# Kernel optimization log

Measured on AMD Instinct MI355X. Metric: run time of the kernel, lower is better.

Reference implementation:

```python
import jax, jax.numpy as jnp
import numpy as np

ALPHAS = [0.1, 0.3, 0.5]
WEIGHTS = [0.5, 0.3, 0.2]


def setup_inputs() -> dict:
    key = jax.random.key(0)
    k1, k2 = jax.random.split(key)
    pred = jax.random.normal(k1, (64, 4096, 64), dtype=jnp.float32)
    target = jax.random.normal(k2, (64, 4096, 64), dtype=jnp.float32)
    return {"pred": pred, "target": target}


def _ema(x, alpha):
    # x: [B, T, D]; EMA along axis 1: y0 = x0, y_t = alpha*x_t + (1-alpha)*y_{t-1}
    x0 = x[:, 0]                      # [B, D]
    xs = jnp.moveaxis(x[:, 1:], 1, 0)  # [T-1, B, D] for scan over time

    def step(carry, xt):
        y = alpha * xt + (1.0 - alpha) * carry
        return y, y

    _, ys = jax.lax.scan(step, x0, xs)  # [T-1, B, D]
    return jnp.concatenate([x0[:, None], jnp.moveaxis(ys, 0, 1)], axis=1)


def reference(pred, target):
    loss = None
    for alpha, weight in zip(ALPHAS, WEIGHTS):
        pe = _ema(pred, alpha)
        te = _ema(target, alpha)
        mse = jnp.mean((pe - te) ** 2, axis=1)  # [B, D]
        term = weight * mse
        loss = term if loss is None else loss + term
    return jnp.mean(loss)  # reduction='mean'
```

## Files before the change

kernel.cpp:

```cpp
#include <hip/hip_runtime.h>


#define T_LEN   4096
#define F_LEN   64
#define NCHUNK  16
#define CHUNK   256
#define WARM    128

__global__ __launch_bounds__(64)
void MultiScaleTrendLoss_910533067632_kernel(const float* __restrict__ pred,
                                             const float* __restrict__ targ,
                                             float* __restrict__ out)
{
    const int f = threadIdx.x;
    const int b = blockIdx.x >> 4;
    const int c = blockIdx.x & (NCHUNK - 1);
    const int t0 = c * CHUNK;

    float e0 = 0.f, e1 = 0.f, e2 = 0.f;
    float s0 = 0.f, s1 = 0.f, s2 = 0.f;

    const int tstart = (c == 0) ? 0 : (t0 - WARM);
    const float* __restrict__ p = pred + ((size_t)b * T_LEN + tstart) * F_LEN + f;
    const float* __restrict__ q = targ + ((size_t)b * T_LEN + tstart) * F_LEN + f;

    if (c == 0) {
        float d = *p - *q; p += F_LEN; q += F_LEN;
        e0 = d; e1 = d; e2 = d;
        float dd = d * d;
        s0 = dd; s1 = dd; s2 = dd;
        #pragma unroll 8
        for (int i = 1; i < CHUNK; ++i) {
            float dv = *p - *q; p += F_LEN; q += F_LEN;
            e0 = fmaf(0.9f, e0, 0.1f * dv);
            e1 = fmaf(0.7f, e1, 0.3f * dv);
            e2 = fmaf(0.5f, e2, 0.5f * dv);
            s0 = fmaf(e0, e0, s0);
            s1 = fmaf(e1, e1, s1);
            s2 = fmaf(e2, e2, s2);
        }
    } else {
        #pragma unroll 8
        for (int i = 0; i < WARM; ++i) {
            float dv = *p - *q; p += F_LEN; q += F_LEN;
            e0 = fmaf(0.9f, e0, 0.1f * dv);
            e1 = fmaf(0.7f, e1, 0.3f * dv);
            e2 = fmaf(0.5f, e2, 0.5f * dv);
        }
        #pragma unroll 8
        for (int i = 0; i < CHUNK; ++i) {
            float dv = *p - *q; p += F_LEN; q += F_LEN;
            e0 = fmaf(0.9f, e0, 0.1f * dv);
            e1 = fmaf(0.7f, e1, 0.3f * dv);
            e2 = fmaf(0.5f, e2, 0.5f * dv);
            s0 = fmaf(e0, e0, s0);
            s1 = fmaf(e1, e1, s1);
            s2 = fmaf(e2, e2, s2);
        }
    }

    float s = 0.5f * s0 + 0.3f * s1 + 0.2f * s2;
    #pragma unroll
    for (int off = 32; off > 0; off >>= 1)
        s += __shfl_down(s, off, 64);

    if (f == 0) {
        atomicAdd(out, s * (1.0f / 16777216.0f));
    }
}

extern "C" void kernel_launch(void* const* d_in, const int* in_sizes, int n_in,
                              void* d_out, int out_size, void* d_ws, size_t ws_size,
                              hipStream_t stream) {
    const float* pred = (const float*)d_in[0];
    const float* targ = (const float*)d_in[1];
    float* out = (float*)d_out;

    hipMemsetAsync(out, 0, sizeof(float) * out_size, stream);

    dim3 grid(64 * NCHUNK);
    dim3 block(64);
    MultiScaleTrendLoss_910533067632_kernel<<<grid, block, 0, stream>>>(pred, targ, out);
}
```

Measured before the change: 162.9 us.

## Replace warm-up EMA chunks with exact two-pass chunked scan combining

Splits the EMA recurrence into independent chunks, each run from a zero state, that record their partial sum of squares, a weighted cross term and their final state. A second kernel stitches the chunks together exactly using closed-form decay constants, so the approximate warm-up overlap re-reads go away. It also loads float2 values with double-buffered register prefetch and raises chunk parallelism. The cost is an extra kernel launch and a workspace round trip, and the fallback path assumes the workspace fits the 32-chunk layout without checking.

```diff
diff --git a/kernel.cpp b/kernel.cpp
--- a/kernel.cpp
+++ b/kernel.cpp
@@ -1,72 +1,137 @@
 #include <hip/hip_runtime.h>
 
 
-#define T_LEN   4096
-#define F_LEN   64
-#define NCHUNK  16
-#define CHUNK   256
-#define WARM    128
+#define T_LEN 4096
+#define F_LEN 64
+#define NB    64
+#define NPAIR 4096
 
+constexpr double powd(double r, int n) {
+    double v = 1.0, b = r;
+    while (n > 0) { if (n & 1) v *= b; b *= b; n >>= 1; }
+    return v;
+}
+
+template<int NCHUNK>
 __global__ __launch_bounds__(64)
-void MultiScaleTrendLoss_910533067632_kernel(const float* __restrict__ pred,
-                                             const float* __restrict__ targ,
-                                             float* __restrict__ out)
+void mstl_pass1(const float2* __restrict__ pred,
+                const float2* __restrict__ targ,
+                float* __restrict__ ws)
 {
-    const int f = threadIdx.x;
-    const int b = blockIdx.x >> 4;
-    const int c = blockIdx.x & (NCHUNK - 1);
-    const int t0 = c * CHUNK;
+    constexpr int CHUNK = T_LEN / NCHUNK;
+    constexpr int NSTG  = CHUNK / 4;
+    constexpr float R0 = 0.9f, R1 = 0.7f, R2 = 0.5f;
+    constexpr float A0 = 0.1f, A1 = 0.3f, A2 = 0.5f;
 
-    float e0 = 0.f, e1 = 0.f, e2 = 0.f;
-    float s0 = 0.f, s1 = 0.f, s2 = 0.f;
+    const int lane = threadIdx.x;
+    const int g    = lane >> 5;
+    const int fh   = lane & 31;
+    const int task = blockIdx.x * 2 + g;
+    const int b    = task / NCHUNK;
+    const int c    = task % NCHUNK;
 
-    const int tstart = (c == 0) ? 0 : (t0 - WARM);
-    const float* __restrict__ p = pred + ((size_t)b * T_LEN + tstart) * F_LEN + f;
-    const float* __restrict__ q = targ + ((size_t)b * T_LEN + tstart) * F_LEN + f;
+    const float2* __restrict__ p = pred + ((size_t)(b * T_LEN + c * CHUNK)) * 32 + fh;
+    const float2* __restrict__ q = targ + ((size_t)(b * T_LEN + c * CHUNK)) * 32 + fh;
 
-    if (c == 0) {
-        float d = *p - *q; p += F_LEN; q += F_LEN;
-        e0 = d; e1 = d; e2 = d;
-        float dd = d * d;
-        s0 = dd; s1 = dd; s2 = dd;
-        #pragma unroll 8
-        for (int i = 1; i < CHUNK; ++i) {
-            float dv = *p - *q; p += F_LEN; q += F_LEN;
-            e0 = fmaf(0.9f, e0, 0.1f * dv);
-            e1 = fmaf(0.7f, e1, 0.3f * dv);
-            e2 = fmaf(0.5f, e2, 0.5f * dv);
-            s0 = fmaf(e0, e0, s0);
-            s1 = fmaf(e1, e1, s1);
-            s2 = fmaf(e2, e2, s2);
-        }
-    } else {
-        #pragma unroll 8
-        for (int i = 0; i < WARM; ++i) {
-            float dv = *p - *q; p += F_LEN; q += F_LEN;
-            e0 = fmaf(0.9f, e0, 0.1f * dv);
-            e1 = fmaf(0.7f, e1, 0.3f * dv);
-            e2 = fmaf(0.5f, e2, 0.5f * dv);
-        }
-        #pragma unroll 8
-        for (int i = 0; i < CHUNK; ++i) {
-            float dv = *p - *q; p += F_LEN; q += F_LEN;
-            e0 = fmaf(0.9f, e0, 0.1f * dv);
-            e1 = fmaf(0.7f, e1, 0.3f * dv);
-            e2 = fmaf(0.5f, e2, 0.5f * dv);
-            s0 = fmaf(e0, e0, s0);
-            s1 = fmaf(e1, e1, s1);
-            s2 = fmaf(e2, e2, s2);
-        }
+    float2 z0{0,0}, z1{0,0}, z2{0,0};
+    float2 a0{0,0}, a1{0,0}, a2{0,0};
+    float2 b0{0,0}, b1{0,0}, b2{0,0};
+    float  w0 = R0, w1 = R1, w2 = R2;
+
+    float2 pA0,pA1,pA2,pA3, qA0,qA1,qA2,qA3;
+    float2 pB0,pB1,pB2,pB3, qB0,qB1,qB2,qB3;
+
+#define LOADA(t0) { pA0=p[(size_t)(t0)*32]; pA1=p[(size_t)((t0)+1)*32]; \
+                    pA2=p[(size_t)((t0)+2)*32]; pA3=p[(size_t)((t0)+3)*32]; \
+                    qA0=q[(size_t)(t0)*32]; qA1=q[(size_t)((t0)+1)*32]; \
+                    qA2=q[(size_t)((t0)+2)*32]; qA3=q[(size_t)((t0)+3)*32]; }
+#define LOADB(t0) { pB0=p[(size_t)(t0)*32]; pB1=p[(size_t)((t0)+1)*32]; \
+                    pB2=p[(size_t)((t0)+2)*32]; pB3=p[(size_t)((t0)+3)*32]; \
+                    qB0=q[(size_t)(t0)*32]; qB1=q[(size_t)((t0)+1)*32]; \
+                    qB2=q[(size_t)((t0)+2)*32]; qB3=q[(size_t)((t0)+3)*32]; }
+#define STEP(pp, qq) { \
+    float dx = (pp).x - (qq).x, dy = (pp).y - (qq).y; \
+    z0.x = fmaf(R0, z0.x, A0*dx); z0.y = fmaf(R0, z0.y, A0*dy); \
+    a0.x = fmaf(z0.x, z0.x, a0.x); a0.y = fmaf(z0.y, z0.y, a0.y); \
+    b0.x = fmaf(z0.x, w0, b0.x);   b0.y = fmaf(z0.y, w0, b0.y);   w0 *= R0; \
+    z1.x = fmaf(R1, z1.x, A1*dx); z1.y = fmaf(R1, z1.y, A1*dy); \
+    a1.x = fmaf(z1.x, z1.x, a1.x); a1.y = fmaf(z1.y, z1.y, a1.y); \
+    b1.x = fmaf(z1.x, w1, b1.x);   b1.y = fmaf(z1.y, w1, b1.y);   w1 *= R1; \
+    z2.x = fmaf(R2, z2.x, A2*dx); z2.y = fmaf(R2, z2.y, A2*dy); \
+    a2.x = fmaf(z2.x, z2.x, a2.x); a2.y = fmaf(z2.y, z2.y, a2.y); \
+    b2.x = fmaf(z2.x, w2, b2.x);   b2.y = fmaf(z2.y, w2, b2.y);   w2 *= R2; }
+#define COMPA() { STEP(pA0,qA0) STEP(pA1,qA1) STEP(pA2,qA2) STEP(pA3,qA3) }
+#define COMPB() { STEP(pB0,qB0) STEP(pB1,qB1) STEP(pB2,qB2) STEP(pB3,qB3) }
+
+    LOADA(0);
+    #pragma unroll
+    for (int s = 0; s < NSTG; s += 2) {
+        LOADB((s + 1) * 4);
+        COMPA();
+        if (s + 2 < NSTG) LOADA((s + 2) * 4);
+        COMPB();
+    }
+#undef LOADA
+#undef LOADB
+#undef STEP
+#undef COMPA
+#undef COMPB
+
+    const int pf = b * F_LEN + fh * 2;
+#define ST(slot, val) *(float2*)(ws + ((size_t)(slot) * NCHUNK + c) * NPAIR + pf) = (val);
+    ST(0, a0) ST(1, b0) ST(2, z0)
+    ST(3, a1) ST(4, b1) ST(5, z1)
+    ST(6, a2) ST(7, b2) ST(8, z2)
+#undef ST
+}
+
+template<int NCHUNK>
+__global__ __launch_bounds__(64)
+void mstl_pass2(const float* __restrict__ ws,
+                const float* __restrict__ pred,
+                const float* __restrict__ targ,
+                float* __restrict__ out)
+{
+    constexpr int CHUNK = T_LEN / NCHUNK;
+    constexpr float RL[3] = { (float)powd(0.9, CHUNK), (float)powd(0.7, CHUNK),
+                              (float)powd(0.5, CHUNK) };
+    constexpr float CC[3] = {
+        (float)(0.81 * (1.0 - powd(0.9, 2*CHUNK)) / (1.0 - 0.81)),
+        (float)(0.49 * (1.0 - powd(0.7, 2*CHUNK)) / (1.0 - 0.49)),
+        (float)(0.25 * (1.0 - powd(0.5, 2*CHUNK)) / (1.0 - 0.25)) };
+    constexpr float WGT[3] = { 0.5f, 0.3f, 0.2f };
+
+    const int a   = blockIdx.x >> 6;
+    const int pfb = blockIdx.x & 63;
+    const int pf  = pfb * 64 + threadIdx.x;
+    const int b   = pf >> 6, f = pf & 63;
+
+    float rl = (a == 0) ? RL[0] : (a == 1) ? RL[1] : RL[2];
+    float cc = (a == 0) ? CC[0] : (a == 1) ? CC[1] : CC[2];
+    float wg = (a == 0) ? WGT[0] : (a == 1) ? WGT[1] : WGT[2];
+
+    const size_t row0 = (size_t)b * T_LEN * F_LEN + f;
+    float e = pred[row0] - targ[row0];
+
+    const float* __restrict__ base = ws + (size_t)(a * 3) * NCHUNK * NPAIR + pf;
+
+    float s = 0.f;
+    #pragma unroll 8
+    for (int c = 0; c < NCHUNK; ++c) {
+        float A = base[((size_t)0 * NCHUNK + c) * NPAIR];
+        float B = base[((size_t)1 * NCHUNK + c) * NPAIR];
+        float Z = base[((size_t)2 * NCHUNK + c) * NPAIR];
+        s += A + e * (2.f * B + e * cc);
+        e = fmaf(rl, e, Z);
     }
 
-    float s = 0.5f * s0 + 0.3f * s1 + 0.2f * s2;
+    float total = s * wg;
     #pragma unroll
     for (int off = 32; off > 0; off >>= 1)
-        s += __shfl_down(s, off, 64);
+        total += __shfl_down(total, off, 64);
 
-    if (f == 0) {
-        atomicAdd(out, s * (1.0f / 16777216.0f));
-    }
+    if (threadIdx.x == 0)
+        atomicAdd(out, total * (1.0f / 16777216.0f));
 }
 
 extern "C" void kernel_launch(void* const* d_in, const int* in_sizes, int n_in,
@@ -75,10 +140,18 @@
     const float* pred = (const float*)d_in[0];
     const float* targ = (const float*)d_in[1];
     float* out = (float*)d_out;
+    float* ws  = (float*)d_ws;
 
     hipMemsetAsync(out, 0, sizeof(float) * out_size, stream);
 
-    dim3 grid(64 * NCHUNK);
-    dim3 block(64);
-    MultiScaleTrendLoss_910533067632_kernel<<<grid, block, 0, stream>>>(pred, targ, out);
+    const size_t need64 = (size_t)9 * 64 * NPAIR * sizeof(float);
+    if (ws_size >= need64) {
+        mstl_pass1<64><<<dim3(NB * 64 / 2), dim3(64), 0, stream>>>(
+            (const float2*)pred, (const float2*)targ, ws);
+        mstl_pass2<64><<<dim3(192), dim3(64), 0, stream>>>(ws, pred, targ, out);
+    } else {
+        mstl_pass1<32><<<dim3(NB * 32 / 2), dim3(64), 0, stream>>>(
+            (const float2*)pred, (const float2*)targ, ws);
+        mstl_pass2<32><<<dim3(192), dim3(64), 0, stream>>>(ws, pred, targ, out);
+    }
 }
```

After: 169.5 us. +4.0%, slower.
